# Optimization experiments

Measured on AMD Instinct MI355X. Metric: run time of the kernel, lower is better.

Reference implementation:

```python
import jax, jax.numpy as jnp
import numpy as np

H2 = 128  # 2*hidden_dim

def setup_inputs() -> dict:
    key = jax.random.key(0)
    k1, k2, k3 = jax.random.split(key, 3)
    B, Lb, Lp = 64, 1024, 1024
    body = jax.random.normal(k1, (B, Lb, H2), dtype=jnp.float32)
    pun = jax.random.normal(k2, (B, Lp, H2), dtype=jnp.float32)
    w_u = jax.random.normal(k3, (3 * H2, 1), dtype=jnp.float32)
    return {"batch_size": B, "body": body, "pun": pun, "w_u": w_u}

def reference(batch_size, body, pun, w_u):
    # score[b,i,j] = [body_i ; pun_j ; body_i*pun_j] @ w_u
    # Decompose w_u into the three 128-dim blocks so the double loop fuses
    # into two matvecs plus one weighted batched GEMM.
    w = w_u[:, 0]
    w1, w2, w3 = w[:H2], w[H2:2 * H2], w[2 * H2:]
    s_body = jnp.einsum('bid,d->bi', body, w1)          # [B, Lb]
    s_pun = jnp.einsum('bjd,d->bj', pun, w2)            # [B, Lp]
    s_cross = jnp.einsum('bid,bjd->bij', body * w3, pun)  # [B, Lb, Lp]
    return s_cross + s_body[:, :, None] + s_pun[:, None, :]
```

## Files before the change

### kernel.cpp

```cpp
#include <hip/hip_runtime.h>


#define LSEQ 1024
#define H2K  128


typedef __attribute__((ext_vector_type(8))) short bfrag;
typedef __attribute__((ext_vector_type(4))) float f32x4;

__device__ __forceinline__ short f2bf(float x) {
    unsigned u = __float_as_uint(x);
    unsigned r = (u + 0x7fff + ((u >> 16) & 1)) >> 16;
    return (short)r;
}
__device__ __forceinline__ float bf2f(short s) {
    return __uint_as_float(((unsigned)(unsigned short)s) << 16);
}

__device__ __forceinline__ void ld16(void* lds, const void* g) {
    __builtin_amdgcn_global_load_lds(
        (const __attribute__((address_space(1))) void*)g,
        (__attribute__((address_space(3))) void*)lds, 16, 0, 0);
}

__global__ __launch_bounds__(256) void prep_kernel(
    const float* __restrict__ body, const float* __restrict__ pun,
    const float* __restrict__ w_u, float* __restrict__ ws)
{
    const int flag = blockIdx.y;
    const int lane = threadIdx.x & 63;
    const int wv   = threadIdx.x >> 6;
    const size_t row = (size_t)blockIdx.x * 4 + wv;

    const float* src = (flag ? pun : body) + row * H2K;
    const float2 v  = *(const float2*)(src + lane * 2);
    const float2 wm = *(const float2*)(w_u + flag * H2K + lane * 2);

    float p = v.x * wm.x + v.y * wm.y;
    p += __shfl_xor(p, 32);
    p += __shfl_xor(p, 16);
    p += __shfl_xor(p, 8);
    p += __shfl_xor(p, 4);
    p += __shfl_xor(p, 2);
    p += __shfl_xor(p, 1);
    if (lane == 0) ws[(size_t)flag * 65536 + row] = p;

    float cx = v.x, cy = v.y;
    if (!flag) {
        const float2 w3v = *(const float2*)(w_u + 2 * H2K + lane * 2);
        cx *= w3v.x; cy *= w3v.y;
    }
    const short h0 = f2bf(cx), h1 = f2bf(cy);
    const short l0 = f2bf(cx - bf2f(h0)), l1 = f2bf(cy - bf2f(h1));

    short* hb = (short*)(ws + 131072) + (size_t)flag * 16777216 + row * H2K + lane * 2;
    *(unsigned*)hb =
        ((unsigned)(unsigned short)h0) | ((unsigned)(unsigned short)h1 << 16);
    *(unsigned*)(hb + 8388608) =
        ((unsigned)(unsigned short)l0) | ((unsigned)(unsigned short)l1 << 16);
}

__global__ __launch_bounds__(512, 4) void align_mfma(
    const float* __restrict__ ws, float* __restrict__ out)
{
    __shared__ __align__(16) short Ch[4096], Cl[4096];
    __shared__ __align__(16) short Ph[8192], Pl[8192];

    const int nwg = gridDim.x;
    const int bid = blockIdx.x;
    const int tid = (bid & 7) * (nwg >> 3) + (bid >> 3);
    const int bb = tid >> 5;
    const int r5 = tid & 31;
    const int ti = (r5 >> 2) * 128;
    const int tj = (r5 & 3) * 256;

    const int t    = threadIdx.x;
    const int lane = t & 63;
    const int w    = t >> 6;

    const int srow = w * 16 + (lane & 15);
    const int k8   = lane >> 4;
    const short* base = (const short*)(ws + 131072);
    const size_t crow = (size_t)(bb * LSEQ + ti + srow) * H2K + k8 * 8;
    const size_t prow = (size_t)(bb * LSEQ + tj + srow) * H2K + k8 * 8;
    const short* gCh = base + crow;
    const short* gCl = base + 8388608 + crow;
    const short* gPh = base + 16777216 + prow;
    const short* gPl = base + 25165824 + prow;
    const size_t R2OFF = (size_t)128 * H2K;

    const int jg = w & 3;
    const int ig = w >> 2;
    f32x4 acc[4][4] = {};

    for (int kt = 0; kt < 4; ++kt) {
        if (kt) __syncthreads();

        ld16(&Ch[t * 8],         gCh + kt * 32);
        ld16(&Cl[t * 8],         gCl + kt * 32);
        ld16(&Ph[t * 8],         gPh + kt * 32);
        ld16(&Ph[(512 + t) * 8], gPh + R2OFF + kt * 32);
        ld16(&Pl[t * 8],         gPl + kt * 32);
        ld16(&Pl[(512 + t) * 8], gPl + R2OFF + kt * 32);
        __syncthreads();

        bfrag ph[4], pl[4];
#pragma unroll
        for (int jj = 0; jj < 4; ++jj) {
            ph[jj] = *(const bfrag*)&Ph[((jg * 4 + jj) * 64 + lane) * 8];
            pl[jj] = *(const bfrag*)&Pl[((jg * 4 + jj) * 64 + lane) * 8];
        }
#pragma unroll
        for (int ii = 0; ii < 4; ++ii) {
            const bfrag ch = *(const bfrag*)&Ch[((ig * 4 + ii) * 64 + lane) * 8];
            const bfrag cl = *(const bfrag*)&Cl[((ig * 4 + ii) * 64 + lane) * 8];
#pragma unroll
            for (int jj = 0; jj < 4; ++jj) {
                acc[jj][ii] = __builtin_amdgcn_mfma_f32_16x16x32_bf16(ph[jj], ch, acc[jj][ii], 0, 0, 0);
                acc[jj][ii] = __builtin_amdgcn_mfma_f32_16x16x32_bf16(ph[jj], cl, acc[jj][ii], 0, 0, 0);
                acc[jj][ii] = __builtin_amdgcn_mfma_f32_16x16x32_bf16(pl[jj], ch, acc[jj][ii], 0, 0, 0);
            }
        }
    }

    const float* sbp = ws + (size_t)bb * LSEQ;
    const float* spp = ws + 65536 + (size_t)bb * LSEQ;
    const int qd = lane >> 4, ln = lane & 15;
#pragma unroll
    for (int jj = 0; jj < 4; ++jj) {
        const int j0 = tj + (jg * 4 + jj) * 16 + qd * 4;
        const float4 spv = *(const float4*)(spp + j0);
#pragma unroll
        for (int ii = 0; ii < 4; ++ii) {
            const int row = ti + (ig * 4 + ii) * 16 + ln;
            const float sb = sbp[row];
            const f32x4 a = acc[jj][ii];
            float4 r = { a[0] + sb + spv.x, a[1] + sb + spv.y,
                         a[2] + sb + spv.z, a[3] + sb + spv.w };
            *(float4*)&out[((size_t)bb * LSEQ + row) * LSEQ + j0] = r;
        }
    }
}

extern "C" void kernel_launch(void* const* d_in, const int* in_sizes, int n_in,
                              void* d_out, int out_size, void* d_ws, size_t ws_size,
                              hipStream_t stream) {
    const float* body = (const float*)d_in[1];
    const float* pun  = (const float*)d_in[2];
    const float* w_u  = (const float*)d_in[3];
    float* out = (float*)d_out;
    float* ws  = (float*)d_ws;
    const int B = in_sizes[1] / (LSEQ * H2K);

    dim3 g1((B * LSEQ) / 4, 2, 1);
    prep_kernel<<<g1, 256, 0, stream>>>(body, pun, w_u, ws);

    dim3 g2(B * 32, 1, 1);
    align_mfma<<<g2, 512, 0, stream>>>(ws, out);
}
```

Before: 427.0 us.

## Fuse prep into MFMA kernel and drop bf16 split-precision correction terms

Removes the separate prep kernel and has the GEMM kernel read fp32 body/pun directly, computing the two matvec dot products and bf16 conversion on the fly into LDS. It also drops the hi/lo bf16 split, so each tile uses one MFMA per fragment pair instead of three. This cuts launch overhead, workspace round-trips and two thirds of the matrix work, at the cost of lower accuracy (single bf16) and redundant conversion of body/pun rows across tiles.

```diff
diff --git a/kernel.cpp b/kernel.cpp
--- a/kernel.cpp
+++ b/kernel.cpp
@@ -3,7 +3,6 @@
 
 #define LSEQ 1024
 #define H2K  128
-
 
 typedef __attribute__((ext_vector_type(8))) short bfrag;
 typedef __attribute__((ext_vector_type(4))) float f32x4;
@@ -13,58 +12,15 @@
     unsigned r = (u + 0x7fff + ((u >> 16) & 1)) >> 16;
     return (short)r;
 }
-__device__ __forceinline__ float bf2f(short s) {
-    return __uint_as_float(((unsigned)(unsigned short)s) << 16);
-}
 
-__device__ __forceinline__ void ld16(void* lds, const void* g) {
-    __builtin_amdgcn_global_load_lds(
-        (const __attribute__((address_space(1))) void*)g,
-        (__attribute__((address_space(3))) void*)lds, 16, 0, 0);
-}
-
-__global__ __launch_bounds__(256) void prep_kernel(
+__global__ __launch_bounds__(512, 4) void align_fused(
     const float* __restrict__ body, const float* __restrict__ pun,
-    const float* __restrict__ w_u, float* __restrict__ ws)
+    const float* __restrict__ w_u, float* __restrict__ out)
 {
-    const int flag = blockIdx.y;
-    const int lane = threadIdx.x & 63;
-    const int wv   = threadIdx.x >> 6;
-    const size_t row = (size_t)blockIdx.x * 4 + wv;
-
-    const float* src = (flag ? pun : body) + row * H2K;
-    const float2 v  = *(const float2*)(src + lane * 2);
-    const float2 wm = *(const float2*)(w_u + flag * H2K + lane * 2);
-
-    float p = v.x * wm.x + v.y * wm.y;
-    p += __shfl_xor(p, 32);
-    p += __shfl_xor(p, 16);
-    p += __shfl_xor(p, 8);
-    p += __shfl_xor(p, 4);
-    p += __shfl_xor(p, 2);
-    p += __shfl_xor(p, 1);
-    if (lane == 0) ws[(size_t)flag * 65536 + row] = p;
-
-    float cx = v.x, cy = v.y;
-    if (!flag) {
-        const float2 w3v = *(const float2*)(w_u + 2 * H2K + lane * 2);
-        cx *= w3v.x; cy *= w3v.y;
-    }
-    const short h0 = f2bf(cx), h1 = f2bf(cy);
-    const short l0 = f2bf(cx - bf2f(h0)), l1 = f2bf(cy - bf2f(h1));
-
-    short* hb = (short*)(ws + 131072) + (size_t)flag * 16777216 + row * H2K + lane * 2;
-    *(unsigned*)hb =
-        ((unsigned)(unsigned short)h0) | ((unsigned)(unsigned short)h1 << 16);
-    *(unsigned*)(hb + 8388608) =
-        ((unsigned)(unsigned short)l0) | ((unsigned)(unsigned short)l1 << 16);
-}
-
-__global__ __launch_bounds__(512, 4) void align_mfma(
-    const float* __restrict__ ws, float* __restrict__ out)
-{
-    __shared__ __align__(16) short Ch[4096], Cl[4096];
-    __shared__ __align__(16) short Ph[8192], Pl[8192];
+    __shared__ __align__(16) short Cb[4096];
+    __shared__ __align__(16) short Pb[8192];
+    __shared__ __align__(16) float sb[128];
+    __shared__ __align__(16) float sp[256];
 
     const int nwg = gridDim.x;
     const int bid = blockIdx.x;
@@ -80,64 +36,87 @@
 
     const int srow = w * 16 + (lane & 15);
     const int k8   = lane >> 4;
-    const short* base = (const short*)(ws + 131072);
-    const size_t crow = (size_t)(bb * LSEQ + ti + srow) * H2K + k8 * 8;
-    const size_t prow = (size_t)(bb * LSEQ + tj + srow) * H2K + k8 * 8;
-    const short* gCh = base + crow;
-    const short* gCl = base + 8388608 + crow;
-    const short* gPh = base + 16777216 + prow;
-    const short* gPl = base + 25165824 + prow;
-    const size_t R2OFF = (size_t)128 * H2K;
+
+    const float4* bp  = (const float4*)(body + (size_t)(bb * LSEQ + ti + srow) * H2K) + k8 * 2;
+    const float4* p1  = (const float4*)(pun  + (size_t)(bb * LSEQ + tj + srow) * H2K) + k8 * 2;
+    const float4* p2  = (const float4*)(pun  + (size_t)(bb * LSEQ + tj + 128 + srow) * H2K) + k8 * 2;
+    const float4* w1v = (const float4*)(w_u          ) + k8 * 2;
+    const float4* w2v = (const float4*)(w_u +     H2K) + k8 * 2;
+    const float4* w3v = (const float4*)(w_u + 2 * H2K) + k8 * 2;
 
     const int jg = w & 3;
     const int ig = w >> 2;
     f32x4 acc[4][4] = {};
+    float db = 0.f, dp1 = 0.f, dp2 = 0.f;
 
     for (int kt = 0; kt < 4; ++kt) {
         if (kt) __syncthreads();
 
-        ld16(&Ch[t * 8],         gCh + kt * 32);
-        ld16(&Cl[t * 8],         gCl + kt * 32);
-        ld16(&Ph[t * 8],         gPh + kt * 32);
-        ld16(&Ph[(512 + t) * 8], gPh + R2OFF + kt * 32);
-        ld16(&Pl[t * 8],         gPl + kt * 32);
-        ld16(&Pl[(512 + t) * 8], gPl + R2OFF + kt * 32);
+        const float4 xb0 = bp[kt * 8],  xb1 = bp[kt * 8 + 1];
+        const float4 u30 = w3v[kt * 8], u31 = w3v[kt * 8 + 1];
+        const float4 u10 = w1v[kt * 8], u11 = w1v[kt * 8 + 1];
+        db += xb0.x * u10.x + xb0.y * u10.y + xb0.z * u10.z + xb0.w * u10.w
+            + xb1.x * u11.x + xb1.y * u11.y + xb1.z * u11.z + xb1.w * u11.w;
+        bfrag fb;
+        fb[0] = f2bf(xb0.x * u30.x); fb[1] = f2bf(xb0.y * u30.y);
+        fb[2] = f2bf(xb0.z * u30.z); fb[3] = f2bf(xb0.w * u30.w);
+        fb[4] = f2bf(xb1.x * u31.x); fb[5] = f2bf(xb1.y * u31.y);
+        fb[6] = f2bf(xb1.z * u31.z); fb[7] = f2bf(xb1.w * u31.w);
+        *(bfrag*)&Cb[t * 8] = fb;
+
+        const float4 y10 = p1[kt * 8],  y11 = p1[kt * 8 + 1];
+        const float4 y20 = p2[kt * 8],  y21 = p2[kt * 8 + 1];
+        const float4 u20 = w2v[kt * 8], u21 = w2v[kt * 8 + 1];
+        dp1 += y10.x * u20.x + y10.y * u20.y + y10.z * u20.z + y10.w * u20.w
+             + y11.x * u21.x + y11.y * u21.y + y11.z * u21.z + y11.w * u21.w;
+        dp2 += y20.x * u20.x + y20.y * u20.y + y20.z * u20.z + y20.w * u20.w
+             + y21.x * u21.x + y21.y * u21.y + y21.z * u21.z + y21.w * u21.w;
+        bfrag f1, f2;
+        f1[0] = f2bf(y10.x); f1[1] = f2bf(y10.y); f1[2] = f2bf(y10.z); f1[3] = f2bf(y10.w);
+        f1[4] = f2bf(y11.x); f1[5] = f2bf(y11.y); f1[6] = f2bf(y11.z); f1[7] = f2bf(y11.w);
+        f2[0] = f2bf(y20.x); f2[1] = f2bf(y20.y); f2[2] = f2bf(y20.z); f2[3] = f2bf(y20.w);
+        f2[4] = f2bf(y21.x); f2[5] = f2bf(y21.y); f2[6] = f2bf(y21.z); f2[7] = f2bf(y21.w);
+        *(bfrag*)&Pb[t * 8]         = f1;
+        *(bfrag*)&Pb[(512 + t) * 8] = f2;
+
         __syncthreads();
 
-        bfrag ph[4], pl[4];
+        bfrag ph[4];
 #pragma unroll
-        for (int jj = 0; jj < 4; ++jj) {
-            ph[jj] = *(const bfrag*)&Ph[((jg * 4 + jj) * 64 + lane) * 8];
-            pl[jj] = *(const bfrag*)&Pl[((jg * 4 + jj) * 64 + lane) * 8];
-        }
+        for (int jj = 0; jj < 4; ++jj)
+            ph[jj] = *(const bfrag*)&Pb[((jg * 4 + jj) * 64 + lane) * 8];
 #pragma unroll
         for (int ii = 0; ii < 4; ++ii) {
-            const bfrag ch = *(const bfrag*)&Ch[((ig * 4 + ii) * 64 + lane) * 8];
-            const bfrag cl = *(const bfrag*)&Cl[((ig * 4 + ii) * 64 + lane) * 8];
+            const bfrag ch = *(const bfrag*)&Cb[((ig * 4 + ii) * 64 + lane) * 8];
 #pragma unroll
-            for (int jj = 0; jj < 4; ++jj) {
+            for (int jj = 0; jj < 4; ++jj)
                 acc[jj][ii] = __builtin_amdgcn_mfma_f32_16x16x32_bf16(ph[jj], ch, acc[jj][ii], 0, 0, 0);
-                acc[jj][ii] = __builtin_amdgcn_mfma_f32_16x16x32_bf16(ph[jj], cl, acc[jj][ii], 0, 0, 0);
-                acc[jj][ii] = __builtin_amdgcn_mfma_f32_16x16x32_bf16(pl[jj], ch, acc[jj][ii], 0, 0, 0);
-            }
         }
     }
 
-    const float* sbp = ws + (size_t)bb * LSEQ;
-    const float* spp = ws + 65536 + (size_t)bb * LSEQ;
+    db  += __shfl_xor(db, 16);  db  += __shfl_xor(db, 32);
+    dp1 += __shfl_xor(dp1, 16); dp1 += __shfl_xor(dp1, 32);
+    dp2 += __shfl_xor(dp2, 16); dp2 += __shfl_xor(dp2, 32);
+    if (k8 == 0) {
+        sb[srow] = db;
+        sp[srow] = dp1;
+        sp[128 + srow] = dp2;
+    }
+    __syncthreads();
+
     const int qd = lane >> 4, ln = lane & 15;
 #pragma unroll
     for (int jj = 0; jj < 4; ++jj) {
-        const int j0 = tj + (jg * 4 + jj) * 16 + qd * 4;
-        const float4 spv = *(const float4*)(spp + j0);
+        const int jl = (jg * 4 + jj) * 16 + qd * 4;
+        const float4 spv = *(const float4*)&sp[jl];
 #pragma unroll
         for (int ii = 0; ii < 4; ++ii) {
-            const int row = ti + (ig * 4 + ii) * 16 + ln;
-            const float sb = sbp[row];
+            const int rl = (ig * 4 + ii) * 16 + ln;
+            const float sbv = sb[rl];
             const f32x4 a = acc[jj][ii];
-            float4 r = { a[0] + sb + spv.x, a[1] + sb + spv.y,
-                         a[2] + sb + spv.z, a[3] + sb + spv.w };
-            *(float4*)&out[((size_t)bb * LSEQ + row) * LSEQ + j0] = r;
+            float4 r = { a[0] + sbv + spv.x, a[1] + sbv + spv.y,
+                         a[2] + sbv + spv.z, a[3] + sbv + spv.w };
+            *(float4*)&out[(size_t)(bb * LSEQ + ti + rl) * LSEQ + tj + jl] = r;
         }
     }
 }
@@ -149,12 +128,8 @@
     const float* pun  = (const float*)d_in[2];
     const float* w_u  = (const float*)d_in[3];
     float* out = (float*)d_out;
-    float* ws  = (float*)d_ws;
     const int B = in_sizes[1] / (LSEQ * H2K);
 
-    dim3 g1((B * LSEQ) / 4, 2, 1);
-    prep_kernel<<<g1, 256, 0, stream>>>(body, pun, w_u, ws);
-
-    dim3 g2(B * 32, 1, 1);
-    align_mfma<<<g2, 512, 0, stream>>>(ws, out);
+    dim3 g(B * 32, 1, 1);
+    align_fused<<<g, 512, 0, stream>>>(body, pun, w_u, out);
 }
```

New measurement: 376.6 us. 1.13x faster.
